# Kernel optimization log

Measured on AMD Instinct MI355X. Metric: run time of the kernel, lower is better.

Reference implementation:

```python
import jax, jax.numpy as jnp
import numpy as np

D_MODEL = 1024
NUM_HEADS = 16
HEAD_DIM = D_MODEL // NUM_HEADS
SCALE = HEAD_DIM ** -0.5


def _split_heads(x):
    # [B, L, D] -> [B, H, L, hd]
    B, L, _ = x.shape
    return x.reshape(B, L, NUM_HEADS, HEAD_DIM).transpose(0, 2, 1, 3)


def setup_inputs() -> dict:
    key = jax.random.key(0)
    ks = jax.random.split(key, 16)
    B, Lq, Lv, P, Lc = 8, 256, 576, 2048, 256
    inp = {
        "query_input": jax.random.normal(ks[0], (B, Lq, D_MODEL), jnp.float32),
        "visual_tokens": jax.random.normal(ks[1], (B, Lv, D_MODEL), jnp.float32),
        "past_key": jax.random.normal(ks[2], (B, NUM_HEADS, P, HEAD_DIM), jnp.float32),
        "past_value": jax.random.normal(ks[3], (B, NUM_HEADS, P, HEAD_DIM), jnp.float32),
        "past_valid_len": jax.random.randint(ks[4], (B,), 0, P + 1, jnp.int32),
        "current_context": jax.random.normal(ks[5], (B, Lc, D_MODEL), jnp.float32),
        "current_valid_mask": jax.random.randint(ks[6], (B, Lc), 0, 2, jnp.int32).astype(jnp.bool_),
    }
    s = 1.0 / np.sqrt(D_MODEL)
    inp["Wq"] = jax.random.normal(ks[7], (D_MODEL, D_MODEL), jnp.float32) * s
    inp["bq"] = jnp.zeros((D_MODEL,), jnp.float32)
    inp["Wk"] = jax.random.normal(ks[8], (D_MODEL, D_MODEL), jnp.float32) * s
    inp["bk"] = jnp.zeros((D_MODEL,), jnp.float32)
    inp["Wv"] = jax.random.normal(ks[9], (D_MODEL, D_MODEL), jnp.float32) * s
    inp["bv"] = jnp.zeros((D_MODEL,), jnp.float32)
    inp["Wo"] = jax.random.normal(ks[10], (D_MODEL, D_MODEL), jnp.float32) * s
    inp["bo"] = jnp.zeros((D_MODEL,), jnp.float32)
    return inp


def reference(query_input, visual_tokens, past_key, past_value, past_valid_len,
              current_context, current_valid_mask, Wq, bq, Wk, bk, Wv, bv, Wo, bo):
    B, Lq, _ = query_input.shape
    P = past_key.shape[2]
    Lv = visual_tokens.shape[1]
    Lc = current_context.shape[1]

    q = _split_heads(query_input @ Wq + bq)                       # [B,H,Lq,hd]
    k_vis = _split_heads(visual_tokens @ Wk + bk)                 # [B,H,Lv,hd]
    v_vis = _split_heads(visual_tokens @ Wv + bv)
    k_cur = _split_heads(current_context @ Wk + bk)               # [B,H,Lc,hd]
    v_cur = _split_heads(current_context @ Wv + bv)

    # padding masks (True = masked); full past length kept, positions >= valid_len masked
    past_mask = jnp.arange(P)[None, :] >= past_valid_len[:, None]  # [B,P]
    vis_mask = jnp.zeros((B, Lv), jnp.bool_)
    cur_mask = ~current_valid_mask                                 # [B,Lc]
    key_padding_mask = jnp.concatenate([vis_mask, past_mask, cur_mask], axis=1)  # [B,K]

    k_full = jnp.concatenate([k_vis, past_key, k_cur], axis=2)    # [B,H,K,hd]
    v_full = jnp.concatenate([v_vis, past_value, v_cur], axis=2)

    scores = jnp.einsum('bhqd,bhkd->bhqk', q, k_full) * SCALE
    neg = jnp.finfo(scores.dtype).min
    scores = jnp.where(key_padding_mask[:, None, None, :], neg, scores)
    attn = jax.nn.softmax(scores, axis=-1)
    out = jnp.einsum('bhqk,bhkd->bhqd', attn, v_full)             # [B,H,Lq,hd]
    out = out.transpose(0, 2, 1, 3).reshape(B, Lq, D_MODEL)
    return out @ Wo + bo
```

## Files before the change

kernel.cpp:

```cpp
#include <hip/hip_runtime.h>

using half8 = __attribute__((ext_vector_type(8))) _Float16;
using f32x4 = __attribute__((ext_vector_type(4))) float;

#define MFMA16(a,b,c) __builtin_amdgcn_mfma_f32_16x16x32_f16((a),(b),(c),0,0,0)

constexpr int DM = 1024;
constexpr int NH = 16;
constexpr int HD = 64;
constexpr int LQ = 256, LV = 576, PP = 2048, LC = 256;
constexpr int KVC = LV + LC;
constexpr int NSPLIT = 8;

__global__ __launch_bounds__(256) void wtrans_k(
    const float* __restrict__ W0, const float* __restrict__ W1,
    const float* __restrict__ W2, const float* __restrict__ W3,
    _Float16* __restrict__ T0, _Float16* __restrict__ T1,
    _Float16* __restrict__ T2, _Float16* __restrict__ T3)
{
  __shared__ float t[64][65];
  const float* W = blockIdx.z==0 ? W0 : blockIdx.z==1 ? W1 : blockIdx.z==2 ? W2 : W3;
  _Float16*   T  = blockIdx.z==0 ? T0 : blockIdx.z==1 ? T1 : blockIdx.z==2 ? T2 : T3;
  const int k0 = blockIdx.x*64, n0 = blockIdx.y*64;
  const int r = threadIdx.x >> 2, c0 = (threadIdx.x & 3)*16;
  const float* src = W + (size_t)(k0+r)*DM + n0 + c0;
  #pragma unroll
  for (int j=0;j<4;++j) {
    f32x4 v = *(const f32x4*)(src + 4*j);
    #pragma unroll
    for (int i=0;i<4;++i) t[r][c0+4*j+i] = v[i];
  }
  __syncthreads();
  half8 o0, o1;
  #pragma unroll
  for (int i=0;i<8;++i) { o0[i] = (_Float16)t[c0+i][r]; o1[i] = (_Float16)t[c0+8+i][r]; }
  _Float16* dst = T + (size_t)(n0+r)*DM + k0 + c0;
  *(half8*)dst = o0;
  *(half8*)(dst+8) = o1;
}

template<bool AF16, int MODE>
__device__ __forceinline__ void gemm_body(
    const void* __restrict__ Av, const _Float16* __restrict__ Wt,
    const float* __restrict__ bias, void* __restrict__ outv,
    int L, int off, int LK, int m0, int n0)
{
  __shared__ __align__(16) _Float16 As[128*40];
  __shared__ __align__(16) _Float16 Bs[128*40];
  const int tid = threadIdx.x;
  const int lane = tid & 63, wid = tid >> 6;
  const int l15 = lane & 15, l4 = lane >> 4;
  const int wm = wid >> 1, wn = wid & 1;
  const int sr = tid >> 1, sc = (tid & 1)*16;

  _Float16 hv[16], wv[16];

  auto loadT = [&](int kt) {
    if constexpr (AF16) {
      const _Float16* ap = (const _Float16*)Av + (size_t)(m0+sr)*DM + kt*32 + sc;
      half8 x = *(const half8*)ap, y = *(const half8*)(ap+8);
      #pragma unroll
      for (int i=0;i<8;++i){ hv[i]=x[i]; hv[8+i]=y[i]; }
    } else {
      const float* ap = (const float*)Av + (size_t)(m0+sr)*DM + kt*32 + sc;
      #pragma unroll
      for (int j=0;j<4;++j){
        f32x4 v = *(const f32x4*)(ap+4*j);
        #pragma unroll
        for (int i=0;i<4;++i) hv[4*j+i] = (_Float16)v[i];
      }
    }
    const _Float16* wp = Wt + (size_t)(n0+sr)*DM + kt*32 + sc;
    half8 x = *(const half8*)wp, y = *(const half8*)(wp+8);
    #pragma unroll
    for (int i=0;i<8;++i){ wv[i]=x[i]; wv[8+i]=y[i]; }
  };

  f32x4 acc[4][4] = {};
  loadT(0);

  for (int kt=0; kt<32; ++kt) {
    __syncthreads();
    {
      half8 a0,a1,b0,b1;
      #pragma unroll
      for (int i=0;i<8;++i){ a0[i]=hv[i]; a1[i]=hv[8+i]; b0[i]=wv[i]; b1[i]=wv[8+i]; }
      *(half8*)&As[sr*40+sc]   = a0;
      *(half8*)&As[sr*40+sc+8] = a1;
      *(half8*)&Bs[sr*40+sc]   = b0;
      *(half8*)&Bs[sr*40+sc+8] = b1;
    }
    __syncthreads();
    if (kt < 31) loadT(kt+1);

    half8 af[4], bf[4];
    #pragma unroll
    for (int mf=0;mf<4;++mf) af[mf] = *(const half8*)&As[(wm*64+mf*16+l15)*40 + l4*8];
    #pragma unroll
    for (int nf=0;nf<4;++nf) bf[nf] = *(const half8*)&Bs[(wn*64+nf*16+l15)*40 + l4*8];
    #pragma unroll
    for (int mf=0;mf<4;++mf)
      #pragma unroll
      for (int nf=0;nf<4;++nf)
        acc[mf][nf] = MFMA16(af[mf], bf[nf], acc[mf][nf]);
  }

  #pragma unroll
  for (int nf=0;nf<4;++nf) {
    const int col = n0 + wn*64 + nf*16 + l15;
    const float bv = bias[col];
    const int hh = col >> 6, dd = col & 63;
    #pragma unroll
    for (int mf=0;mf<4;++mf) {
      const int rbase = m0 + wm*64 + mf*16 + l4*4;
      #pragma unroll
      for (int r=0;r<4;++r) {
        const int t = rbase + r;
        const float v = acc[mf][nf][r] + bv;
        if constexpr (MODE==0) {
          const int bb = t / L, pos = t - bb*L;
          ((_Float16*)outv)[ ((size_t)((bb*NH + hh)*LK + off + pos))*HD + dd ] = (_Float16)v;
        } else {
          ((float*)outv)[ (size_t)t*DM + col ] = v;
        }
      }
    }
  }
}

__global__ __launch_bounds__(256) void proj_k(
    const float* __restrict__ qin, const float* __restrict__ vis, const float* __restrict__ cur,
    const _Float16* __restrict__ Wtq, const _Float16* __restrict__ Wtk, const _Float16* __restrict__ Wtv,
    const float* __restrict__ bq, const float* __restrict__ bk, const float* __restrict__ bv,
    _Float16* __restrict__ qhp, _Float16* __restrict__ kvcp, _Float16* __restrict__ vvcp)
{
  const int bx = blockIdx.x, by = blockIdx.y;
  const float* A; const _Float16* Wt; const float* bias; _Float16* out;
  int m0, n0, L, off, LK;
  if (bx < 16) {
    if (by >= 8) return;
    A = qin; m0 = bx*128; L = LQ; off = 0; LK = LQ;
    Wt = Wtq; bias = bq; out = qhp; n0 = by*128;
  } else {
    if (bx < 52) { A = vis; m0 = (bx-16)*128; L = LV; off = 0; }
    else         { A = cur; m0 = (bx-52)*128; L = LC; off = LV; }
    LK = KVC;
    if (by < 8) { Wt = Wtk; bias = bk; out = kvcp; n0 = by*128; }
    else        { Wt = Wtv; bias = bv; out = vvcp; n0 = (by-8)*128; }
  }
  gemm_body<false,0>(A, Wt, bias, out, L, off, LK, m0, n0);
}

__global__ __launch_bounds__(256) void gemmo_k(
    const _Float16* __restrict__ A, const _Float16* __restrict__ Wt,
    const float* __restrict__ bias, float* __restrict__ out)
{
  gemm_body<true,1>(A, Wt, bias, out, 1, 0, 0, blockIdx.x*128, blockIdx.y*128);
}

__global__ __launch_bounds__(512) void attn_k(
  const _Float16* __restrict__ qh, const _Float16* __restrict__ kvc,
  const _Float16* __restrict__ vvc, const float* __restrict__ pk,
  const float* __restrict__ pv, const int* __restrict__ pvl,
  const int* __restrict__ cvm, _Float16* __restrict__ Opart,
  float* __restrict__ mpart, float* __restrict__ lpart)
{
  __shared__ __align__(16) _Float16 Ks[64*72];
  __shared__ __align__(16) _Float16 Vs[64*72];
  __shared__ float mk[64];
  __shared__ __align__(16) _Float16 Ps[8][16*72];

  const int bh = blockIdx.x;
  const int ck = blockIdx.y;
  const int b = bh >> 4;
  const int tid = threadIdx.x;
  const int lane = tid & 63, wid = tid >> 6;
  const int l15 = lane & 15, l4 = lane >> 4;

  const int myvl = pvl[b];
  const int vpt = (myvl + 63) >> 6;
  const int T = 9 + vpt + 4;
  const int qn = T >> 3, rr = T & 7;
  const int len = qn + (ck < rr ? 1 : 0);
  const int lo = ck*qn + (ck < rr ? ck : rr);
  const int hi = lo + len;

  half8 aq[2][2];
  {
    const _Float16* qb = qh + ((size_t)bh*LQ + wid*32)*HD;
    #pragma unroll
    for (int rb=0;rb<2;++rb)
      #pragma unroll
      for (int kc=0;kc<2;++kc) {
        half8 x = *(const half8*)(qb + (rb*16+l15)*HD + kc*32 + l4*8);
        #pragma unroll
        for (int j=0;j<8;++j) x[j] = x[j] * (_Float16)0.125f;
        aq[rb][kc] = x;
      }
  }

  f32x4 accO[2][4] = {};
  float mrun[2][4], lrun[2][4];
  #pragma unroll
  for (int rb=0;rb<2;++rb)
    #pragma unroll
    for (int r=0;r<4;++r){ mrun[rb][r] = -3.0e38f; lrun[rb][r] = 0.f; }

  const int skey = tid >> 3;
  const int sd   = (tid & 7) * 8;
  const int vswz = (tid & 7) << 3;
  const int skeyv = skey ^ vswz;

  half8 kreg, vreg;
  f32x4 k0r, k1r, v0r, v1r;
  float mreg = 0.f;
  int ptype = 0;

  auto prefetch = [&](int t) {
    int s;
    if (t < 9)            { ptype = 0; s = t*64; }
    else if (t < 9 + vpt) { ptype = 1; s = (t-9)*64; }
    else                  { ptype = 2; s = LV + (t-9-vpt)*64; }
    if (ptype != 1) {
      const _Float16* kp = kvc + ((size_t)bh*KVC + s)*HD;
      const _Float16* vp = vvc + ((size_t)bh*KVC + s)*HD;
      kreg = *(const half8*)(kp + skey*HD + sd);
      vreg = *(const half8*)(vp + skey*HD + sd);
      if (tid < 64) mreg = (ptype==2) ? (cvm[b*LC + (s - LV) + tid] ? 0.f : -1e30f) : 0.f;
    } else {
      const float* kp = pk + ((size_t)bh*PP + s)*HD;
      const float* vp = pv + ((size_t)bh*PP + s)*HD;
      k0r = *(const f32x4*)(kp + skey*HD + sd);
      k1r = *(const f32x4*)(kp + skey*HD + sd + 4);
      v0r = *(const f32x4*)(vp + skey*HD + sd);
      v1r = *(const f32x4*)(vp + skey*HD + sd + 4);
      if (tid < 64) mreg = (s + tid < myvl) ? 0.f : -1e30f;
    }
  };

  prefetch(lo);

  for (int t=lo; t<hi; ++t) {
    __syncthreads();
    if (ptype != 1) {
      *(half8*)&Ks[skey*72 + sd] = kreg;
      #pragma unroll
      for (int j=0;j<8;++j) Vs[(sd+j)*72 + skeyv] = vreg[j];
    } else {
      half8 kx;
      #pragma unroll
      for (int i=0;i<4;++i){ kx[i] = (_Float16)k0r[i]; kx[4+i] = (_Float16)k1r[i]; }
      *(half8*)&Ks[skey*72 + sd] = kx;
      #pragma unroll
      for (int j=0;j<4;++j) Vs[(sd+j)*72 + skeyv]   = (_Float16)v0r[j];
      #pragma unroll
      for (int j=0;j<4;++j) Vs[(sd+4+j)*72 + skeyv] = (_Float16)v1r[j];
    }
    if (tid < 64) mk[tid] = mreg;
    __syncthreads();
    if (t+1 < hi) prefetch(t+1);

    half8 bk_[4][2];
    #pragma unroll
    for (int nf=0;nf<4;++nf)
      #pragma unroll
      for (int kc=0;kc<2;++kc)
        bk_[nf][kc] = *(const half8*)&Ks[(nf*16+l15)*72 + kc*32 + l4*8];
    f32x4 sf[2][4] = {};
    #pragma unroll
    for (int rb=0;rb<2;++rb)
      #pragma unroll
      for (int nf=0;nf<4;++nf)
        #pragma unroll
        for (int kc=0;kc<2;++kc)
          sf[rb][nf] = MFMA16(aq[rb][kc], bk_[nf][kc], sf[rb][nf]);

    float mc[4];
    #pragma unroll
    for (int nf=0;nf<4;++nf) mc[nf] = mk[nf*16 + l15];
    #pragma unroll
    for (int rb=0;rb<2;++rb)
      #pragma unroll
      for (int nf=0;nf<4;++nf)
        #pragma unroll
        for (int r=0;r<4;++r)
          sf[rb][nf][r] += mc[nf];

    #pragma unroll
    for (int rb=0;rb<2;++rb)
      #pragma unroll
      for (int r=0;r<4;++r) {
        float mx = fmaxf(fmaxf(sf[rb][0][r],sf[rb][1][r]), fmaxf(sf[rb][2][r],sf[rb][3][r]));
        mx = fmaxf(mx, __shfl_xor(mx,1));
        mx = fmaxf(mx, __shfl_xor(mx,2));
        mx = fmaxf(mx, __shfl_xor(mx,4));
        mx = fmaxf(mx, __shfl_xor(mx,8));
        const float mn = fmaxf(mrun[rb][r], mx);
        const float al = __expf(mrun[rb][r] - mn);
        float rs = 0.f;
        #pragma unroll
        for (int nf=0;nf<4;++nf){ float p = __expf(sf[rb][nf][r]-mn); sf[rb][nf][r]=p; rs+=p; }
        rs += __shfl_xor(rs,1);
        rs += __shfl_xor(rs,2);
        rs += __shfl_xor(rs,4);
        rs += __shfl_xor(rs,8);
        lrun[rb][r] = lrun[rb][r]*al + rs;
        mrun[rb][r] = mn;
        #pragma unroll
        for (int df=0;df<4;++df) accO[rb][df][r] *= al;
      }

    half8 bvv[4][2];
    #pragma unroll
    for (int df=0;df<4;++df) {
      const int rot = (df*2 + (l15>>3)) & 7;
      #pragma unroll
      for (int kc=0;kc<2;++kc)
        bvv[df][kc] = *(const half8*)&Vs[(df*16+l15)*72 + ((((kc<<2)|l4) ^ rot) << 3)];
    }

    _Float16* pw = &Ps[wid][0];
    #pragma unroll
    for (int rb=0;rb<2;++rb) {
      #pragma unroll
      for (int nf=0;nf<4;++nf)
        #pragma unroll
        for (int r=0;r<4;++r)
          pw[(l4*4 + r)*72 + nf*16 + l15] = (_Float16)sf[rb][nf][r];

      half8 ap[2];
      #pragma unroll
      for (int kc=0;kc<2;++kc)
        ap[kc] = *(const half8*)&pw[l15*72 + kc*32 + l4*8];

      #pragma unroll
      for (int df=0;df<4;++df)
        #pragma unroll
        for (int kc=0;kc<2;++kc)
          accO[rb][df] = MFMA16(ap[kc], bvv[df][kc], accO[rb][df]);
    }
  }

  const int base = (ck*128 + bh) * LQ;
  #pragma unroll
  for (int rb=0;rb<2;++rb)
    #pragma unroll
    for (int r=0;r<4;++r) {
      const int row = wid*32 + rb*16 + l4*4 + r;
      #pragma unroll
      for (int df=0;df<4;++df)
        Opart[((size_t)(base + row))*HD + df*16 + l15] = (_Float16)accO[rb][df][r];
      if (l15 == 0) {
        mpart[base + row] = mrun[rb][r];
        lpart[base + row] = lrun[rb][r];
      }
    }
}

__global__ __launch_bounds__(256) void combine_k(
    const _Float16* __restrict__ Opart, const float* __restrict__ mpart,
    const float* __restrict__ lpart, _Float16* __restrict__ aout)
{
  const int t = blockIdx.x*256 + threadIdx.x;
  const int rg = t >> 3;
  const int d0 = (t & 7) * 8;
  const int bh = rg >> 8, qr = rg & 255;
  const int b = bh >> 4, h = bh & 15;

  float m[NSPLIT], l[NSPLIT];
  float mstar = -3.0e38f;
  #pragma unroll
  for (int c=0;c<NSPLIT;++c) {
    m[c] = mpart[(c*128 + bh)*LQ + qr];
    l[c] = lpart[(c*128 + bh)*LQ + qr];
    mstar = fmaxf(mstar, m[c]);
  }
  float lsum = 0.f, w[NSPLIT];
  #pragma unroll
  for (int c=0;c<NSPLIT;++c) { w[c] = __expf(m[c]-mstar); lsum += l[c]*w[c]; }
  const float inv = 1.f / lsum;

  float o[8] = {};
  #pragma unroll
  for (int c=0;c<NSPLIT;++c) {
    half8 x = *(const half8*)&Opart[((size_t)((c*128 + bh)*LQ + qr))*HD + d0];
    #pragma unroll
    for (int i=0;i<8;++i) o[i] += (float)x[i]*w[c];
  }
  half8 y;
  #pragma unroll
  for (int i=0;i<8;++i) y[i] = (_Float16)(o[i]*inv);
  *(half8*)(aout + ((size_t)(b*LQ + qr))*DM + h*HD + d0) = y;
}

extern "C" void kernel_launch(void* const* d_in, const int* in_sizes, int n_in,
                              void* d_out, int out_size, void* d_ws, size_t ws_size,
                              hipStream_t stream)
{
  const float* qin = (const float*)d_in[0];
  const float* vis = (const float*)d_in[1];
  const float* pk  = (const float*)d_in[2];
  const float* pv  = (const float*)d_in[3];
  const int*   pvl = (const int*)d_in[4];
  const float* cur = (const float*)d_in[5];
  const int*   cvm = (const int*)d_in[6];
  const float* Wq = (const float*)d_in[7];  const float* bq = (const float*)d_in[8];
  const float* Wk = (const float*)d_in[9];  const float* bk = (const float*)d_in[10];
  const float* Wv = (const float*)d_in[11]; const float* bv = (const float*)d_in[12];
  const float* Wo = (const float*)d_in[13]; const float* bo = (const float*)d_in[14];

  char* ws = (char*)d_ws;
  _Float16* Wtq  = (_Float16*)(ws + ((size_t) 0<<20));
  _Float16* Wtk  = (_Float16*)(ws + ((size_t) 2<<20));
  _Float16* Wtv  = (_Float16*)(ws + ((size_t) 4<<20));
  _Float16* Wto  = (_Float16*)(ws + ((size_t) 6<<20));
  _Float16* qhp  = (_Float16*)(ws + ((size_t) 8<<20));
  _Float16* kvcp = (_Float16*)(ws + ((size_t)12<<20));
  _Float16* vvcp = (_Float16*)(ws + ((size_t)26<<20));
  _Float16* aoutp= (_Float16*)(ws + ((size_t)40<<20));
  _Float16* Opart= (_Float16*)(ws + ((size_t)45<<20));
  float*    mpart= (float*)   (ws + ((size_t)77<<20));
  float*    lpart= (float*)   (ws + ((size_t)78<<20));

  wtrans_k<<<dim3(16,16,4), 256, 0, stream>>>(Wq,Wk,Wv,Wo, Wtq,Wtk,Wtv,Wto);

  proj_k<<<dim3(68,16), 256, 0, stream>>>(qin, vis, cur, Wtq, Wtk, Wtv,
                                          bq, bk, bv, qhp, kvcp, vvcp);

  attn_k<<<dim3(128,NSPLIT), 512, 0, stream>>>(qhp, kvcp, vvcp, pk, pv, pvl, cvm,
                                               Opart, mpart, lpart);

  combine_k<<<dim3(1024), 256, 0, stream>>>(Opart, mpart, lpart, aoutp);

  gemmo_k<<<dim3(16,8), 256, 0, stream>>>(aoutp, Wto, bo, (float*)d_out);
}
```

Baseline: 351.4 us.

## Pre-convert activations to fp16 and stage GEMM tiles via direct global-to-LDS loads

```diff
diff --git a/kernel.cpp b/kernel.cpp
--- a/kernel.cpp
+++ b/kernel.cpp
@@ -12,6 +12,31 @@
 constexpr int KVC = LV + LC;
 constexpr int NSPLIT = 8;
 
+__device__ __forceinline__ void gload16(const _Float16* g, _Float16* l) {
+  __builtin_amdgcn_global_load_lds(
+      (const __attribute__((address_space(1))) unsigned int*)g,
+      (__attribute__((address_space(3))) unsigned int*)l,
+      16, 0, 0);
+}
+
+__global__ __launch_bounds__(256) void conv_k(
+    const float* __restrict__ q, const float* __restrict__ v, const float* __restrict__ c,
+    _Float16* __restrict__ qo, _Float16* __restrict__ vo, _Float16* __restrict__ co)
+{
+  const int a = blockIdx.y;
+  const float* src = a==0 ? q : a==1 ? v : c;
+  _Float16*   dst  = a==0 ? qo : a==1 ? vo : co;
+  const int n = (a==1) ? 8*LV*DM : 8*LQ*DM;
+  const int i = (blockIdx.x*256 + threadIdx.x) * 8;
+  if (i >= n) return;
+  f32x4 x0 = *(const f32x4*)(src+i);
+  f32x4 x1 = *(const f32x4*)(src+i+4);
+  half8 y;
+  #pragma unroll
+  for (int j=0;j<4;++j){ y[j]=(_Float16)x0[j]; y[4+j]=(_Float16)x1[j]; }
+  *(half8*)(dst+i) = y;
+}
+
 __global__ __launch_bounds__(256) void wtrans_k(
     const float* __restrict__ W0, const float* __restrict__ W1,
     const float* __restrict__ W2, const float* __restrict__ W3,
@@ -39,70 +64,58 @@
   *(half8*)(dst+8) = o1;
 }
 
-template<bool AF16, int MODE>
-__device__ __forceinline__ void gemm_body(
-    const void* __restrict__ Av, const _Float16* __restrict__ Wt,
+template<int MODE>
+__device__ __forceinline__ void gemm16_body(
+    const _Float16* __restrict__ Af, const _Float16* __restrict__ Wt,
     const float* __restrict__ bias, void* __restrict__ outv,
     int L, int off, int LK, int m0, int n0)
 {
-  __shared__ __align__(16) _Float16 As[128*40];
-  __shared__ __align__(16) _Float16 Bs[128*40];
+  __shared__ __align__(16) _Float16 As[128*64];
+  __shared__ __align__(16) _Float16 Bs[128*64];
   const int tid = threadIdx.x;
   const int lane = tid & 63, wid = tid >> 6;
   const int l15 = lane & 15, l4 = lane >> 4;
   const int wm = wid >> 1, wn = wid & 1;
-  const int sr = tid >> 1, sc = (tid & 1)*16;
-
-  _Float16 hv[16], wv[16];
-
-  auto loadT = [&](int kt) {
-    if constexpr (AF16) {
-      const _Float16* ap = (const _Float16*)Av + (size_t)(m0+sr)*DM + kt*32 + sc;
-      half8 x = *(const half8*)ap, y = *(const half8*)(ap+8);
-      #pragma unroll
-      for (int i=0;i<8;++i){ hv[i]=x[i]; hv[8+i]=y[i]; }
-    } else {
-      const float* ap = (const float*)Av + (size_t)(m0+sr)*DM + kt*32 + sc;
-      #pragma unroll
-      for (int j=0;j<4;++j){
-        f32x4 v = *(const f32x4*)(ap+4*j);
-        #pragma unroll
-        for (int i=0;i<4;++i) hv[4*j+i] = (_Float16)v[i];
+  const int lrow = lane >> 3;
+  const int lc8  = lane & 7;
+
+  auto stage = [&](int kt) {
+    #pragma unroll
+    for (int s8 = 0; s8 < 4; ++s8) {
+      const int seg = wid*4 + s8;
+      const int row = seg*8 + lrow;
+      const int c8  = lc8 ^ (row & 7);
+      const size_t gc = (size_t)kt*64 + c8*8;
+      gload16(Af + (size_t)(m0+row)*DM + gc, &As[seg*512]);
+      gload16(Wt + (size_t)(n0+row)*DM + gc, &Bs[seg*512]);
+    }
+  };
+
+  f32x4 acc[4][4] = {};
+  stage(0);
+
+  for (int kt=0; kt<16; ++kt) {
+    __syncthreads();
+    half8 af[4][2], bf[4][2];
+    #pragma unroll
+    for (int mf=0; mf<4; ++mf) {
+      const int ra = wm*64 + mf*16 + l15;
+      const int rb = wn*64 + mf*16 + l15;
+      #pragma unroll
+      for (int kc=0; kc<2; ++kc) {
+        const int g8 = kc*4 + l4;
+        af[mf][kc] = *(const half8*)&As[ra*64 + ((g8 ^ (ra&7))<<3)];
+        bf[mf][kc] = *(const half8*)&Bs[rb*64 + ((g8 ^ (rb&7))<<3)];
       }
     }
-    const _Float16* wp = Wt + (size_t)(n0+sr)*DM + kt*32 + sc;
-    half8 x = *(const half8*)wp, y = *(const half8*)(wp+8);
-    #pragma unroll
-    for (int i=0;i<8;++i){ wv[i]=x[i]; wv[8+i]=y[i]; }
-  };
-
-  f32x4 acc[4][4] = {};
-  loadT(0);
-
-  for (int kt=0; kt<32; ++kt) {
-    __syncthreads();
-    {
-      half8 a0,a1,b0,b1;
-      #pragma unroll
-      for (int i=0;i<8;++i){ a0[i]=hv[i]; a1[i]=hv[8+i]; b0[i]=wv[i]; b1[i]=wv[8+i]; }
-      *(half8*)&As[sr*40+sc]   = a0;
-      *(half8*)&As[sr*40+sc+8] = a1;
-      *(half8*)&Bs[sr*40+sc]   = b0;
-      *(half8*)&Bs[sr*40+sc+8] = b1;
-    }
-    __syncthreads();
-    if (kt < 31) loadT(kt+1);
-
-    half8 af[4], bf[4];
-    #pragma unroll
-    for (int mf=0;mf<4;++mf) af[mf] = *(const half8*)&As[(wm*64+mf*16+l15)*40 + l4*8];
-    #pragma unroll
-    for (int nf=0;nf<4;++nf) bf[nf] = *(const half8*)&Bs[(wn*64+nf*16+l15)*40 + l4*8];
     #pragma unroll
     for (int mf=0;mf<4;++mf)
       #pragma unroll
       for (int nf=0;nf<4;++nf)
-        acc[mf][nf] = MFMA16(af[mf], bf[nf], acc[mf][nf]);
+        #pragma unroll
+        for (int kc=0;kc<2;++kc)
+          acc[mf][nf] = MFMA16(af[mf][kc], bf[nf][kc], acc[mf][nf]);
+    if (kt < 15) { __syncthreads(); stage(kt+1); }
   }
 
   #pragma unroll
@@ -129,33 +142,33 @@
 }
 
 __global__ __launch_bounds__(256) void proj_k(
-    const float* __restrict__ qin, const float* __restrict__ vis, const float* __restrict__ cur,
+    const _Float16* __restrict__ qf, const _Float16* __restrict__ vf, const _Float16* __restrict__ cf,
     const _Float16* __restrict__ Wtq, const _Float16* __restrict__ Wtk, const _Float16* __restrict__ Wtv,
     const float* __restrict__ bq, const float* __restrict__ bk, const float* __restrict__ bv,
     _Float16* __restrict__ qhp, _Float16* __restrict__ kvcp, _Float16* __restrict__ vvcp)
 {
   const int bx = blockIdx.x, by = blockIdx.y;
-  const float* A; const _Float16* Wt; const float* bias; _Float16* out;
+  const _Float16* A; const _Float16* Wt; const float* bias; _Float16* out;
   int m0, n0, L, off, LK;
   if (bx < 16) {
     if (by >= 8) return;
-    A = qin; m0 = bx*128; L = LQ; off = 0; LK = LQ;
+    A = qf; m0 = bx*128; L = LQ; off = 0; LK = LQ;
     Wt = Wtq; bias = bq; out = qhp; n0 = by*128;
   } else {
-    if (bx < 52) { A = vis; m0 = (bx-16)*128; L = LV; off = 0; }
-    else         { A = cur; m0 = (bx-52)*128; L = LC; off = LV; }
+    if (bx < 52) { A = vf; m0 = (bx-16)*128; L = LV; off = 0; }
+    else         { A = cf; m0 = (bx-52)*128; L = LC; off = LV; }
     LK = KVC;
     if (by < 8) { Wt = Wtk; bias = bk; out = kvcp; n0 = by*128; }
     else        { Wt = Wtv; bias = bv; out = vvcp; n0 = (by-8)*128; }
   }
-  gemm_body<false,0>(A, Wt, bias, out, L, off, LK, m0, n0);
+  gemm16_body<0>(A, Wt, bias, out, L, off, LK, m0, n0);
 }
 
 __global__ __launch_bounds__(256) void gemmo_k(
     const _Float16* __restrict__ A, const _Float16* __restrict__ Wt,
     const float* __restrict__ bias, float* __restrict__ out)
 {
-  gemm_body<true,1>(A, Wt, bias, out, 1, 0, 0, blockIdx.x*128, blockIdx.y*128);
+  gemm16_body<1>(A, Wt, bias, out, 1, 0, 0, blockIdx.x*128, blockIdx.y*128);
 }
 
 __global__ __launch_bounds__(512) void attn_k(
@@ -421,10 +434,15 @@
   _Float16* Opart= (_Float16*)(ws + ((size_t)45<<20));
   float*    mpart= (float*)   (ws + ((size_t)77<<20));
   float*    lpart= (float*)   (ws + ((size_t)78<<20));
+  _Float16* qf16 = (_Float16*)(ws + ((size_t)45<<20));
+  _Float16* vf16 = (_Float16*)(ws + ((size_t)50<<20));
+  _Float16* cf16 = (_Float16*)(ws + ((size_t)60<<20));
+
+  conv_k<<<dim3(2304,3), 256, 0, stream>>>(qin, vis, cur, qf16, vf16, cf16);
 
   wtrans_k<<<dim3(16,16,4), 256, 0, stream>>>(Wq,Wk,Wv,Wo, Wtq,Wtk,Wtv,Wto);
 
-  proj_k<<<dim3(68,16), 256, 0, stream>>>(qin, vis, cur, Wtq, Wtk, Wtv,
+  proj_k<<<dim3(68,16), 256, 0, stream>>>(qf16, vf16, cf16, Wtq, Wtk, Wtv,
                                           bq, bk, bv, qhp, kvcp, vvcp);
 
   attn_k<<<dim3(128,NSPLIT), 512, 0, stream>>>(qhp, kvcp, vvcp, pk, pv, pvl, cvm,
```

After: 323.8 us. -7.8%, faster.
